# Performance work log

Hardware: AMD Instinct MI355X
Metric: run time of the kernel (lower is better)

The kernel has to match this reference:

```python
import jax, jax.numpy as jnp
import numpy as np

N = 20000      # nodes
E = 320000     # edges (before self loops)
HID = 128      # args.hidden
HEADS = 8
C1 = HID // 2  # 64, gat1 out per head -> 512 concat
C2 = HID // 4  # 32, gat2 out per head -> 256 concat
D1 = HEADS * C1  # 512
D2 = HEADS * C2  # 256
JKD = HID + D1 + D2  # 896


def _glorot(key, shape):
    fan_in, fan_out = shape[0], shape[-1]
    s = jnp.sqrt(6.0 / (fan_in + fan_out))
    return jax.random.uniform(key, shape, jnp.float32, -s, s)


def setup_inputs() -> dict:
    key = jax.random.key(0)
    ks = jax.random.split(key, 18)
    x = jax.random.normal(ks[0], (N, HID), jnp.float32)
    edge_index = jax.random.randint(ks[1], (2, E), 0, N, dtype=jnp.int32)
    return {
        "x": x,
        "edge_index": edge_index,
        # GATv2 layer 1
        "Wl1": _glorot(ks[2], (HID, D1)), "bl1": jnp.zeros((D1,), jnp.float32),
        "Wr1": _glorot(ks[3], (HID, D1)), "br1": jnp.zeros((D1,), jnp.float32),
        "att1": _glorot(ks[4], (HEADS, C1)),
        "bias1": jnp.zeros((D1,), jnp.float32),
        # GATv2 layer 2
        "Wl2": _glorot(ks[5], (D1, D2)), "bl2": jnp.zeros((D2,), jnp.float32),
        "Wr2": _glorot(ks[6], (D1, D2)), "br2": jnp.zeros((D2,), jnp.float32),
        "att2": _glorot(ks[7], (HEADS, C2)),
        "bias2": jnp.zeros((D2,), jnp.float32),
        # JK linear
        "Wjk": _glorot(ks[8], (JKD, HID)), "bjk": jnp.zeros((HID,), jnp.float32),
    }


def gatv2_layer(x, src, dst, Wl, bl, Wr, br, att, bias, n):
    """PyG GATv2Conv (concat=True, eval mode: no dropout), neg_slope=0.2."""
    H, C = att.shape
    xl = (x @ Wl + bl).reshape(n, H, C)  # source transform (messages)
    xr = (x @ Wr + br).reshape(n, H, C)  # target transform
    e = jax.nn.leaky_relu(xl[src] + xr[dst], 0.2)        # [E,H,C]
    logits = jnp.einsum('ehc,hc->eh', e, att)            # [E,H]
    # numerically stable segment softmax over incoming edges per dst node
    m = jax.ops.segment_max(logits, dst, num_segments=n) # [N,H]
    a = jnp.exp(logits - m[dst])
    denom = jax.ops.segment_sum(a, dst, num_segments=n)
    alpha = a / denom[dst]                               # [E,H]
    out = jax.ops.segment_sum(alpha[:, :, None] * xl[src], dst, num_segments=n)
    return out.reshape(n, H * C) + bias


def reference(x, edge_index, Wl1, bl1, Wr1, br1, att1, bias1,
              Wl2, bl2, Wr2, br2, att2, bias2, Wjk, bjk):
    n = x.shape[0]
    loop = jnp.arange(n, dtype=edge_index.dtype)
    src = jnp.concatenate([edge_index[0], loop])  # add self loops (PyG default)
    dst = jnp.concatenate([edge_index[1], loop])

    jk0 = x
    h1 = jax.nn.elu(gatv2_layer(x, src, dst, Wl1, bl1, Wr1, br1, att1, bias1, n))
    h2 = jax.nn.elu(gatv2_layer(h1, src, dst, Wl2, bl2, Wr2, br2, att2, bias2, n))
    jk = jnp.concatenate([jk0, h1, h2], axis=-1)  # JumpingKnowledge('cat')
    return jk @ Wjk + bjk
```

## Files before the change

### kernel.cpp

```cpp
#include <hip/hip_runtime.h>

typedef unsigned short u16;
typedef __attribute__((ext_vector_type(8))) short bf16x8;
typedef __attribute__((ext_vector_type(4))) float f32x4;

__device__ __forceinline__ float bf2f(u16 u) { return __uint_as_float(((unsigned)u) << 16); }
__device__ __forceinline__ u16 f2bf(float f) {
  unsigned u = __float_as_uint(f);
  u += 0x7fffu + ((u >> 16) & 1u);
  return (u16)(u >> 16);
}
__device__ __forceinline__ void bf2x2(unsigned w, float& lo, float& hi) {
  lo = __uint_as_float(w << 16);
  hi = __uint_as_float(w & 0xffff0000u);
}

__global__ __launch_bounds__(256) void prep_kernel(
    const float* __restrict__ x,
    const float* __restrict__ bl1, const float* __restrict__ br1,
    const float* __restrict__ bl2, const float* __restrict__ br2,
    u16* __restrict__ XH, float* __restrict__ BC1, float* __restrict__ BC2,
    int nx, int total)
{
  int i = blockIdx.x * 256 + threadIdx.x;
  if (i >= total) return;
  if (i < nx) { XH[i] = f2bf(x[i]); return; }
  int j = i - nx;
  if (j < 1024) { BC1[j] = (j < 512) ? bl1[j] : br1[j - 512]; return; }
  int t = j - 1024;
  BC2[t] = (t < 256) ? bl2[t] : br2[t - 256];
}

__global__ __launch_bounds__(256) void wtrans_kernel(
    const float* __restrict__ Wl1, const float* __restrict__ Wr1,
    const float* __restrict__ Wl2, const float* __restrict__ Wr2,
    const float* __restrict__ Wjk,
    u16* __restrict__ Wp)
{
  __shared__ float T[64][65];
  int t = blockIdx.x;
  const float *Wa, *Wb; int Nhalf, lds, k0, n0, KsT, SUBS; size_t obase; bool split;
  if (t < 32) {
    int kt = t & 1, nt = t >> 1;
    k0 = kt * 64; n0 = nt * 64; obase = 0; KsT = 4; SUBS = 8; split = true;
    Wa = Wl1; Wb = Wr1; Nhalf = 512; lds = 512;
  } else if (t < 96) {
    int tt = t - 32; int kt = tt & 7, nt = tt >> 3;
    k0 = kt * 64; n0 = nt * 64; obase = 262144; KsT = 16; SUBS = 8; split = true;
    Wa = Wl2; Wb = Wr2; Nhalf = 256; lds = 256;
  } else {
    int tt = t - 96; int kt = tt % 14, nt = tt / 14;
    k0 = kt * 64; n0 = nt * 64; obase = 786432; KsT = 28; SUBS = 4; split = false;
    Wa = Wjk; Wb = nullptr; Nhalf = 128; lds = 128;
  }
  const int tid = threadIdx.x;
  const int lane = tid & 63, unit = tid >> 6;
  {
    int n = n0 + lane;
    const float* S = (n < Nhalf) ? Wa : Wb;
    int nn = (n < Nhalf) ? n : n - Nhalf;
#pragma unroll
    for (int r = 0; r < 16; ++r) {
      int kl = unit + 4 * r;
      T[kl][lane] = S[(size_t)(k0 + kl) * lds + nn];
    }
  }
  __syncthreads();
  const int tn = n0 >> 6;
#pragma unroll
  for (int u = 0; u < 2; ++u) {
    int c = unit * 2 + u;
    int ks_l = c >> 2, nc = c & 3;
    int ksg = (k0 >> 5) + ks_l;
    size_t ob = obase + ((size_t)(tn * KsT + ksg) * SUBS + nc) * 512 + lane * 8;
#pragma unroll
    for (int j = 0; j < 8; ++j) {
      float v = T[ks_l * 32 + (lane >> 4) * 8 + j][nc * 16 + (lane & 15)];
      u16 h = f2bf(v);
      Wp[ob + j] = h;
      if (split) Wp[ob + 2048 + j] = f2bf(v - bf2f(h));
    }
  }
}

__global__ __launch_bounds__(256) void hist_kernel(
    const int* __restrict__ ei, int E, int ET, int* __restrict__ cnt)
{
  int e = blockIdx.x * 256 + threadIdx.x;
  if (e >= ET) return;
  int d = (e < E) ? ei[E + e] : (e - E);
  atomicAdd(&cnt[d], 1);
}

__global__ __launch_bounds__(1024) void scan_kernel(
    const int* __restrict__ cnt, int* __restrict__ rowptr, int n)
{
  __shared__ int wsum[16];
  __shared__ int carry;
  const int tid = threadIdx.x, lane = tid & 63, wv = tid >> 6;
  if (tid == 0) carry = 0;
  __syncthreads();
  for (int base = 0; base < n; base += 1024) {
    int i = base + tid;
    int v = (i < n) ? cnt[i] : 0;
    int s = v;
#pragma unroll
    for (int ofs = 1; ofs < 64; ofs <<= 1) {
      int t = __shfl_up(s, ofs);
      if (lane >= ofs) s += t;
    }
    if (lane == 63) wsum[wv] = s;
    __syncthreads();
    if (wv == 0 && lane < 16) {
      int t = wsum[lane];
#pragma unroll
      for (int ofs = 1; ofs < 16; ofs <<= 1) {
        int u = __shfl_up(t, ofs);
        if (lane >= ofs) t += u;
      }
      wsum[lane] = t;
    }
    __syncthreads();
    int waveoff = (wv == 0) ? 0 : wsum[wv - 1];
    if (i < n) rowptr[i] = carry + waveoff + s - v;
    int tot = wsum[15];
    __syncthreads();
    if (tid == 0) carry += tot;
    __syncthreads();
  }
  if (threadIdx.x == 0) rowptr[n] = carry;
}

__global__ __launch_bounds__(256) void scatter_kernel(
    const int* __restrict__ ei, int E, int ET,
    const int* __restrict__ rowptr, int* __restrict__ cur, int* __restrict__ srcs)
{
  int e = blockIdx.x * 256 + threadIdx.x;
  if (e >= ET) return;
  int s, d;
  if (e < E) { s = ei[e]; d = ei[E + e]; } else { s = e - E; d = s; }
  int pos = rowptr[d] + atomicAdd(&cur[d], 1);
  srcs[pos] = s;
}

template<int MROWS, int NW, int WPE, bool SPLIT, bool BF16OUT, int LDSU16>
__global__ __launch_bounds__(NW * 64, WPE) void gemmct_kernel(
    const u16* __restrict__ A0, int lda0, int K0,
    const u16* __restrict__ A1, int lda1, int K1,
    const u16* __restrict__ A2, int lda2, int K2,
    const u16* __restrict__ Wp, int KsT,
    int kof0, int kof1, int kof2,
    const float* __restrict__ bias,
    void* __restrict__ Cv, int ldc, int M, int N)
{
  constexpr int SUBS = SPLIT ? 8 : 4;
  __shared__ u16 ldsA[LDSU16];
  const int tid  = threadIdx.x;
  const int lane = tid & 63;
  const int wv   = tid >> 6;
  const int quad = lane >> 4;
  const int r16  = lane & 15;
  const int m0   = blockIdx.x * MROWS;

  const u16* As[3]   = {A0, A1, A2};
  const int  Ks[3]   = {K0, K1, K2};
  const int  ldas[3] = {lda0, lda1, lda2};
  const int  kofs[3] = {kof0, kof1, kof2};

  int soff[3];
  int so = 0;
#pragma unroll
  for (int s = 0; s < 3; ++s) {
    const int K = Ks[s];
    soff[s] = so;
    if (K == 0) continue;
    const int stride = K + 8;
    const int cpr = K >> 3;
    const int sh  = 32 - __clz(cpr - 1);
    const int tot = MROWS << sh;
    for (int c = tid; c < tot; c += NW * 64) {
      int row = c >> sh, kc = c & ((1 << sh) - 1);
      if (kc < cpr) {
        int sr = m0 + row; if (sr >= M) sr = M - 1;
        uint4 v = *reinterpret_cast<const uint4*>(As[s] + (size_t)sr * ldas[s] + kc * 8);
        *reinterpret_cast<uint4*>(&ldsA[so + row * stride + kc * 8]) = v;
      }
    }
    so += MROWS * stride;
  }
  __syncthreads();

  constexpr int MM = MROWS / 16;
  for (int n0w = wv * 64; n0w < N; n0w += NW * 64) {
    const int t = n0w >> 6;
    f32x4 acc[MM][4];
#pragma unroll
    for (int mm = 0; mm < MM; ++mm)
#pragma unroll
      for (int nc = 0; nc < 4; ++nc) acc[mm][nc] = (f32x4){0.f, 0.f, 0.f, 0.f};

#pragma unroll
    for (int s = 0; s < 3; ++s) {
      const int K = Ks[s];
      if (K == 0) continue;
      const int stride = K + 8;
      const int ksb = kofs[s] >> 5;
      const u16* lbase = &ldsA[soff[s] + r16 * stride + quad * 8];

#pragma unroll 2
      for (int k0 = 0; k0 < K; k0 += 32) {
        const int ks = ksb + (k0 >> 5);
        const u16* ch = Wp + (((size_t)(t * KsT + ks) * SUBS) << 9) + lane * 8;
        bf16x8 af[MM];
#pragma unroll
        for (int mm = 0; mm < MM; ++mm)
          af[mm] = *reinterpret_cast<const bf16x8*>(lbase + mm * 16 * stride + k0);
        bf16x8 whf[4], wlf[4];
#pragma unroll
        for (int nc = 0; nc < 4; ++nc) {
          whf[nc] = *reinterpret_cast<const bf16x8*>(ch + (nc << 9));
          if (SPLIT) wlf[nc] = *reinterpret_cast<const bf16x8*>(ch + ((4 + nc) << 9));
        }
#pragma unroll
        for (int mm = 0; mm < MM; ++mm)
#pragma unroll
          for (int nc = 0; nc < 4; ++nc) {
            acc[mm][nc] = __builtin_amdgcn_mfma_f32_16x16x32_bf16(whf[nc], af[mm], acc[mm][nc], 0, 0, 0);
            if (SPLIT)
              acc[mm][nc] = __builtin_amdgcn_mfma_f32_16x16x32_bf16(wlf[nc], af[mm], acc[mm][nc], 0, 0, 0);
          }
      }
    }

#pragma unroll
    for (int mm = 0; mm < MM; ++mm) {
      const int m = m0 + mm * 16 + r16;
      if (m >= M) continue;
#pragma unroll
      for (int nc = 0; nc < 4; ++nc) {
        const int n = n0w + nc * 16 + quad * 4;
        float b0 = 0.f, b1 = 0.f, b2 = 0.f, b3 = 0.f;
        if (bias) {
          float4 bv = *reinterpret_cast<const float4*>(bias + n);
          b0 = bv.x; b1 = bv.y; b2 = bv.z; b3 = bv.w;
        }
        float v0 = acc[mm][nc][0] + b0;
        float v1 = acc[mm][nc][1] + b1;
        float v2 = acc[mm][nc][2] + b2;
        float v3 = acc[mm][nc][3] + b3;
        if (BF16OUT) {
          ushort4 o = { f2bf(v0), f2bf(v1), f2bf(v2), f2bf(v3) };
          *reinterpret_cast<ushort4*>((u16*)Cv + (size_t)m * ldc + n) = o;
        } else {
          float4 o = { v0, v1, v2, v3 };
          *reinterpret_cast<float4*>((float*)Cv + (size_t)m * ldc + n) = o;
        }
      }
    }
  }
}

template<int VPL>
__device__ __forceinline__ void load_row(const u16* p, float* dst) {
  if constexpr (VPL == 8) {
    uint4 t = *reinterpret_cast<const uint4*>(p);
    bf2x2(t.x, dst[0], dst[1]); bf2x2(t.y, dst[2], dst[3]);
    bf2x2(t.z, dst[4], dst[5]); bf2x2(t.w, dst[6], dst[7]);
  } else {
    uint2 t = *reinterpret_cast<const uint2*>(p);
    bf2x2(t.x, dst[0], dst[1]); bf2x2(t.y, dst[2], dst[3]);
  }
}

template<int C>
__global__ __launch_bounds__(256) void gat_node_kernel(
    const u16* __restrict__ XLR,
    const int* __restrict__ rowptr, const int* __restrict__ srcs,
    const float* __restrict__ att, const float* __restrict__ bias,
    u16* __restrict__ Hh, int Nn)
{
  constexpr int D = C * 8;
  constexpr int VPL = D / 64;
  const int lane = threadIdx.x & 63;
  const int wv  = (blockIdx.x * 256 + threadIdx.x) >> 6;
  const int nwv = (gridDim.x * 256) >> 6;

  float c1[VPL], c2[VPL], biasR[VPL];
#pragma unroll
  for (int w = 0; w < VPL; ++w) {
    float a = att[lane * VPL + w];
    c1[w] = 0.6f * a;
    c2[w] = 0.4f * a;
    biasR[w] = bias[lane * VPL + w];
  }

  for (int d = wv; d < Nn; d += nwv) {
    float xr[VPL];
    load_row<VPL>(XLR + (size_t)d * (2 * D) + D + lane * VPL, xr);

    const int jb = rowptr[d], je = rowptr[d + 1];

    float acc[VPL];
    load_row<VPL>(XLR + (size_t)srcs[jb] * (2 * D) + lane * VPL, acc);
    float p0 = 0.f;
#pragma unroll
    for (int w = 0; w < VPL; ++w) {
      float v = acc[w] + xr[w];
      p0 = fmaf(c1[w], v, fmaf(c2[w], fabsf(v), p0));
    }
    p0 += __shfl_xor(p0, 1);
    p0 += __shfl_xor(p0, 2);
    p0 += __shfl_xor(p0, 4);
    float den = 1.f;

    int j = jb + 1;
    for (; j + 3 < je; j += 4) {
      float xa[VPL], xb[VPL], xc[VPL], xd[VPL];
      load_row<VPL>(XLR + (size_t)srcs[j]     * (2 * D) + lane * VPL, xa);
      load_row<VPL>(XLR + (size_t)srcs[j + 1] * (2 * D) + lane * VPL, xb);
      load_row<VPL>(XLR + (size_t)srcs[j + 2] * (2 * D) + lane * VPL, xc);
      load_row<VPL>(XLR + (size_t)srcs[j + 3] * (2 * D) + lane * VPL, xd);
      float pa = 0.f, pb = 0.f, pc = 0.f, pd = 0.f;
#pragma unroll
      for (int w = 0; w < VPL; ++w) {
        float va = xa[w] + xr[w];
        float vb = xb[w] + xr[w];
        float vc = xc[w] + xr[w];
        float vd = xd[w] + xr[w];
        pa = fmaf(c1[w], va, fmaf(c2[w], fabsf(va), pa));
        pb = fmaf(c1[w], vb, fmaf(c2[w], fabsf(vb), pb));
        pc = fmaf(c1[w], vc, fmaf(c2[w], fabsf(vc), pc));
        pd = fmaf(c1[w], vd, fmaf(c2[w], fabsf(vd), pd));
      }
      pa += __shfl_xor(pa, 1); pb += __shfl_xor(pb, 1);
      pc += __shfl_xor(pc, 1); pd += __shfl_xor(pd, 1);
      pa += __shfl_xor(pa, 2); pb += __shfl_xor(pb, 2);
      pc += __shfl_xor(pc, 2); pd += __shfl_xor(pd, 2);
      pa += __shfl_xor(pa, 4); pb += __shfl_xor(pb, 4);
      pc += __shfl_xor(pc, 4); pd += __shfl_xor(pd, 4);
      const float ea = __expf(pa - p0);
      const float eb = __expf(pb - p0);
      const float ec = __expf(pc - p0);
      const float ed = __expf(pd - p0);
      den += (ea + eb) + (ec + ed);
#pragma unroll
      for (int w = 0; w < VPL; ++w) {
        float t0 = fmaf(ea, xa[w], fmaf(eb, xb[w], acc[w]));
        acc[w] = fmaf(ec, xc[w], fmaf(ed, xd[w], t0));
      }
    }
    if (j + 1 < je) {
      float xa[VPL], xb[VPL];
      load_row<VPL>(XLR + (size_t)srcs[j]     * (2 * D) + lane * VPL, xa);
      load_row<VPL>(XLR + (size_t)srcs[j + 1] * (2 * D) + lane * VPL, xb);
      float pa = 0.f, pb = 0.f;
#pragma unroll
      for (int w = 0; w < VPL; ++w) {
        float va = xa[w] + xr[w];
        float vb = xb[w] + xr[w];
        pa = fmaf(c1[w], va, fmaf(c2[w], fabsf(va), pa));
        pb = fmaf(c1[w], vb, fmaf(c2[w], fabsf(vb), pb));
      }
      pa += __shfl_xor(pa, 1); pb += __shfl_xor(pb, 1);
      pa += __shfl_xor(pa, 2); pb += __shfl_xor(pb, 2);
      pa += __shfl_xor(pa, 4); pb += __shfl_xor(pb, 4);
      const float ea = __expf(pa - p0);
      const float eb = __expf(pb - p0);
      den += ea + eb;
#pragma unroll
      for (int w = 0; w < VPL; ++w)
        acc[w] = fmaf(ea, xa[w], fmaf(eb, xb[w], acc[w]));
      j += 2;
    }
    if (j < je) {
      float xa[VPL];
      load_row<VPL>(XLR + (size_t)srcs[j] * (2 * D) + lane * VPL, xa);
      float pa = 0.f;
#pragma unroll
      for (int w = 0; w < VPL; ++w) {
        float va = xa[w] + xr[w];
        pa = fmaf(c1[w], va, fmaf(c2[w], fabsf(va), pa));
      }
      pa += __shfl_xor(pa, 1);
      pa += __shfl_xor(pa, 2);
      pa += __shfl_xor(pa, 4);
      const float ea = __expf(pa - p0);
      den += ea;
#pragma unroll
      for (int w = 0; w < VPL; ++w) acc[w] = fmaf(ea, xa[w], acc[w]);
    }

    const float inv = 1.f / den;
    u16* hh = Hh + (size_t)d * D + lane * VPL;
#pragma unroll
    for (int w = 0; w < VPL; ++w) {
      float v = fmaf(acc[w], inv, biasR[w]);
      v = v > 0.f ? v : (__expf(v) - 1.f);
      hh[w] = f2bf(v);
    }
  }
}


extern "C" void kernel_launch(void* const* d_in, const int* in_sizes, int n_in,
                              void* d_out, int out_size, void* d_ws, size_t ws_size,
                              hipStream_t stream) {
  const float* x     = (const float*)d_in[0];
  const int*   ei    = (const int*)d_in[1];
  const float* Wl1   = (const float*)d_in[2];
  const float* bl1   = (const float*)d_in[3];
  const float* Wr1   = (const float*)d_in[4];
  const float* br1   = (const float*)d_in[5];
  const float* att1  = (const float*)d_in[6];
  const float* bias1 = (const float*)d_in[7];
  const float* Wl2   = (const float*)d_in[8];
  const float* bl2   = (const float*)d_in[9];
  const float* Wr2   = (const float*)d_in[10];
  const float* br2   = (const float*)d_in[11];
  const float* att2  = (const float*)d_in[12];
  const float* bias2 = (const float*)d_in[13];
  const float* Wjk   = (const float*)d_in[14];
  const float* bjk   = (const float*)d_in[15];
  float* out = (float*)d_out;

  const int Nn = in_sizes[0] / 128;
  const int E  = in_sizes[1] / 2;
  const int ET = E + Nn;

  const size_t nx = (size_t)Nn * 128;

  const size_t oW1  = 0;
  const size_t oW2  = 262144;
  const size_t oWjk = 786432;
  const size_t npack = 901120;

  char* ws = (char*)d_ws;
  size_t off = 0;
  u16* XH = (u16*)(ws + off); off += nx * 2;
  u16* Wp = (u16*)(ws + off); off += npack * 2;
  float* BC1 = (float*)(ws + off); off += 1024 * 4;
  float* BC2 = (float*)(ws + off); off += 512 * 4;
  u16* XLR1 = (u16*)(ws + off);
  u16* XLR2 = XLR1;
  off += (size_t)Nn * 1024 * 2;
  u16* H1h = (u16*)(ws + off); off += (size_t)Nn * 512 * 2;
  u16* H2h = (u16*)(ws + off); off += (size_t)Nn * 256 * 2;
  int* rowptr = (int*)(ws + off); off += (size_t)(Nn + 1) * 4;
  int* cur    = (int*)(ws + off); off += (size_t)Nn * 4;
  int* srcs   = (int*)(ws + off); off += (size_t)ET * 4;

  const int nodeblocks = 5000;

  const int nprep = (int)(nx + 1536);
  prep_kernel<<<(nprep + 255) / 256, 256, 0, stream>>>(
      x, bl1, br1, bl2, br2, XH, BC1, BC2, (int)nx, nprep);
  wtrans_kernel<<<124, 256, 0, stream>>>(Wl1, Wr1, Wl2, Wr2, Wjk, Wp);
  hipMemsetAsync(cur, 0, (size_t)Nn * 4, stream);
  hist_kernel<<<(ET + 255) / 256, 256, 0, stream>>>(ei, E, ET, cur);
  scan_kernel<<<1, 1024, 0, stream>>>(cur, rowptr, Nn);
  hipMemsetAsync(cur, 0, (size_t)Nn * 4, stream);
  scatter_kernel<<<(ET + 255) / 256, 256, 0, stream>>>(ei, E, ET, rowptr, cur, srcs);

  gemmct_kernel<32, 8, 4, true, true, 32 * 136>
      <<<(Nn + 31) / 32, 512, 0, stream>>>(
      XH, 128, 128, nullptr, 0, 0, nullptr, 0, 0,
      Wp + oW1, 4, 0, 0, 0, BC1,
      XLR1, 1024, Nn, 1024);
  gat_node_kernel<64><<<nodeblocks, 256, 0, stream>>>(
      XLR1, rowptr, srcs, att1, bias1, H1h, Nn);

  gemmct_kernel<48, 8, 4, true, true, 48 * 520>
      <<<(Nn + 47) / 48, 512, 0, stream>>>(
      H1h, 512, 512, nullptr, 0, 0, nullptr, 0, 0,
      Wp + oW2, 16, 0, 0, 0, BC2,
      XLR2, 512, Nn, 512);
  gat_node_kernel<32><<<nodeblocks, 256, 0, stream>>>(
      XLR2, rowptr, srcs, att2, bias2, H2h, Nn);

  gemmct_kernel<16, 2, 1, false, false, 16 * 920>
      <<<(Nn + 15) / 16, 128, 0, stream>>>(
      XH, 128, 128, H1h, 512, 512, H2h, 256, 256,
      Wp + oWjk, 28, 0, 128, 640, bjk,
      out, 128, Nn, 128);
}
```

Measured before the change: 321.3 us.

## Fuse prep/weight/scatter launches and split GAT aggregation per head

Merges the prep and weight-transpose kernels into one launch that also zeroes the degree counters. The scan now resets the counters itself, and the edge scatter runs as extra blocks inside the first GEMM launch. Together these remove two memsets and two kernel launches. The GAT aggregation kernels are rewritten so that each block handles one head and each node is processed by a small group of 8 or 4 lanes rather than a whole wave, using ds_swizzle reductions and packed 16-byte stores. The tradeoff is more per-node divergence within a wave and repeated rowptr/srcs reads once per head.

After: 298.9 us. 7.0% less time.

```diff
diff --git a/kernel.cpp b/kernel.cpp
--- a/kernel.cpp
+++ b/kernel.cpp
@@ -14,31 +14,45 @@
   lo = __uint_as_float(w << 16);
   hi = __uint_as_float(w & 0xffff0000u);
 }
-
-__global__ __launch_bounds__(256) void prep_kernel(
+__device__ __forceinline__ unsigned pk2(float lo, float hi) {
+  return (unsigned)f2bf(lo) | ((unsigned)f2bf(hi) << 16);
+}
+
+__device__ __forceinline__ float red8(float p) {
+  p += __int_as_float(__builtin_amdgcn_ds_swizzle(__float_as_int(p), 0x041F));
+  p += __int_as_float(__builtin_amdgcn_ds_swizzle(__float_as_int(p), 0x081F));
+  p += __int_as_float(__builtin_amdgcn_ds_swizzle(__float_as_int(p), 0x101F));
+  return p;
+}
+__device__ __forceinline__ float red4(float p) {
+  p += __int_as_float(__builtin_amdgcn_ds_swizzle(__float_as_int(p), 0x041F));
+  p += __int_as_float(__builtin_amdgcn_ds_swizzle(__float_as_int(p), 0x081F));
+  return p;
+}
+
+__global__ __launch_bounds__(256) void prepw_kernel(
     const float* __restrict__ x,
     const float* __restrict__ bl1, const float* __restrict__ br1,
     const float* __restrict__ bl2, const float* __restrict__ br2,
-    u16* __restrict__ XH, float* __restrict__ BC1, float* __restrict__ BC2,
-    int nx, int total)
-{
-  int i = blockIdx.x * 256 + threadIdx.x;
-  if (i >= total) return;
-  if (i < nx) { XH[i] = f2bf(x[i]); return; }
-  int j = i - nx;
-  if (j < 1024) { BC1[j] = (j < 512) ? bl1[j] : br1[j - 512]; return; }
-  int t = j - 1024;
-  BC2[t] = (t < 256) ? bl2[t] : br2[t - 256];
-}
-
-__global__ __launch_bounds__(256) void wtrans_kernel(
     const float* __restrict__ Wl1, const float* __restrict__ Wr1,
     const float* __restrict__ Wl2, const float* __restrict__ Wr2,
     const float* __restrict__ Wjk,
-    u16* __restrict__ Wp)
-{
+    u16* __restrict__ XH, float* __restrict__ BC1, float* __restrict__ BC2,
+    int* __restrict__ cur, u16* __restrict__ Wp,
+    int nx, int total, int prepBlocks)
+{
+  if (blockIdx.x < prepBlocks) {
+    int i = blockIdx.x * 256 + threadIdx.x;
+    if (i >= total) return;
+    if (i < nx) { XH[i] = f2bf(x[i]); return; }
+    int j = i - nx;
+    if (j < 1024) { BC1[j] = (j < 512) ? bl1[j] : br1[j - 512]; return; }
+    if (j < 1536) { int t = j - 1024; BC2[t] = (t < 256) ? bl2[t] : br2[t - 256]; return; }
+    cur[j - 1536] = 0;
+    return;
+  }
   __shared__ float T[64][65];
-  int t = blockIdx.x;
+  int t = blockIdx.x - prepBlocks;
   const float *Wa, *Wb; int Nhalf, lds, k0, n0, KsT, SUBS; size_t obase; bool split;
   if (t < 32) {
     int kt = t & 1, nt = t >> 1;
@@ -93,7 +107,7 @@
 }
 
 __global__ __launch_bounds__(1024) void scan_kernel(
-    const int* __restrict__ cnt, int* __restrict__ rowptr, int n)
+    int* __restrict__ cnt, int* __restrict__ rowptr, int n)
 {
   __shared__ int wsum[16];
   __shared__ int carry;
@@ -103,6 +117,7 @@
   for (int base = 0; base < n; base += 1024) {
     int i = base + tid;
     int v = (i < n) ? cnt[i] : 0;
+    if (i < n) cnt[i] = 0;
     int s = v;
 #pragma unroll
     for (int ofs = 1; ofs < 64; ofs <<= 1) {
@@ -131,20 +146,9 @@
   if (threadIdx.x == 0) rowptr[n] = carry;
 }
 
-__global__ __launch_bounds__(256) void scatter_kernel(
-    const int* __restrict__ ei, int E, int ET,
-    const int* __restrict__ rowptr, int* __restrict__ cur, int* __restrict__ srcs)
-{
-  int e = blockIdx.x * 256 + threadIdx.x;
-  if (e >= ET) return;
-  int s, d;
-  if (e < E) { s = ei[e]; d = ei[E + e]; } else { s = e - E; d = s; }
-  int pos = rowptr[d] + atomicAdd(&cur[d], 1);
-  srcs[pos] = s;
-}
-
-template<int MROWS, int NW, int WPE, bool SPLIT, bool BF16OUT, int LDSU16>
-__global__ __launch_bounds__(NW * 64, WPE) void gemmct_kernel(
+template<int MROWS, int NW, bool SPLIT, bool BF16OUT>
+__device__ __forceinline__ void gemmct_body(
+    u16* __restrict__ ldsA, int bid,
     const u16* __restrict__ A0, int lda0, int K0,
     const u16* __restrict__ A1, int lda1, int K1,
     const u16* __restrict__ A2, int lda2, int K2,
@@ -154,13 +158,12 @@
     void* __restrict__ Cv, int ldc, int M, int N)
 {
   constexpr int SUBS = SPLIT ? 8 : 4;
-  __shared__ u16 ldsA[LDSU16];
   const int tid  = threadIdx.x;
   const int lane = tid & 63;
   const int wv   = tid >> 6;
   const int quad = lane >> 4;
   const int r16  = lane & 15;
-  const int m0   = blockIdx.x * MROWS;
+  const int m0   = bid * MROWS;
 
   const u16* As[3]   = {A0, A1, A2};
   const int  Ks[3]   = {K0, K1, K2};
@@ -260,6 +263,46 @@
   }
 }
 
+template<int MROWS, int NW, int WPE, bool SPLIT, bool BF16OUT, int LDSU16>
+__global__ __launch_bounds__(NW * 64, WPE) void gemmct_kernel(
+    const u16* __restrict__ A0, int lda0, int K0,
+    const u16* __restrict__ A1, int lda1, int K1,
+    const u16* __restrict__ A2, int lda2, int K2,
+    const u16* __restrict__ Wp, int KsT,
+    int kof0, int kof1, int kof2,
+    const float* __restrict__ bias,
+    void* __restrict__ Cv, int ldc, int M, int N)
+{
+  __shared__ u16 ldsA[LDSU16];
+  gemmct_body<MROWS, NW, SPLIT, BF16OUT>(
+      ldsA, blockIdx.x, A0, lda0, K0, A1, lda1, K1, A2, lda2, K2,
+      Wp, KsT, kof0, kof1, kof2, bias, Cv, ldc, M, N);
+}
+
+template<int MROWS, int NW, int WPE, bool SPLIT, bool BF16OUT, int LDSU16>
+__global__ __launch_bounds__(NW * 64, WPE) void gemm1_scatter_kernel(
+    const u16* __restrict__ A0, int lda0, int K0,
+    const u16* __restrict__ Wp, int KsT,
+    const float* __restrict__ bias,
+    void* __restrict__ Cv, int ldc, int M, int N, int gemmBlocks,
+    const int* __restrict__ ei, int E, int ET,
+    const int* __restrict__ rowptr, int* __restrict__ cur, int* __restrict__ srcs)
+{
+  __shared__ u16 ldsA[LDSU16];
+  if ((int)blockIdx.x < gemmBlocks) {
+    gemmct_body<MROWS, NW, SPLIT, BF16OUT>(
+        ldsA, blockIdx.x, A0, lda0, K0, nullptr, 0, 0, nullptr, 0, 0,
+        Wp, KsT, 0, 0, 0, bias, Cv, ldc, M, N);
+    return;
+  }
+  int e = ((int)blockIdx.x - gemmBlocks) * (NW * 64) + (int)threadIdx.x;
+  if (e >= ET) return;
+  int s, d;
+  if (e < E) { s = ei[e]; d = ei[E + e]; } else { s = e - E; d = s; }
+  int pos = rowptr[d] + atomicAdd(&cur[d], 1);
+  srcs[pos] = s;
+}
+
 template<int VPL>
 __device__ __forceinline__ void load_row(const u16* p, float* dst) {
   if constexpr (VPL == 8) {
@@ -272,132 +315,181 @@
   }
 }
 
-template<int C>
-__global__ __launch_bounds__(256) void gat_node_kernel(
+__global__ __launch_bounds__(256) void gath1_kernel(
     const u16* __restrict__ XLR,
     const int* __restrict__ rowptr, const int* __restrict__ srcs,
     const float* __restrict__ att, const float* __restrict__ bias,
     u16* __restrict__ Hh, int Nn)
 {
-  constexpr int D = C * 8;
-  constexpr int VPL = D / 64;
-  const int lane = threadIdx.x & 63;
-  const int wv  = (blockIdx.x * 256 + threadIdx.x) >> 6;
-  const int nwv = (gridDim.x * 256) >> 6;
-
-  float c1[VPL], c2[VPL], biasR[VPL];
-#pragma unroll
-  for (int w = 0; w < VPL; ++w) {
-    float a = att[lane * VPL + w];
+  const int tid   = threadIdx.x;
+  const int s     = tid & 7;
+  const int gib   = tid >> 3;
+  const int head  = blockIdx.x & 7;
+  const int chunk = blockIdx.x >> 3;
+  const int nch   = gridDim.x >> 3;
+
+  const int hoff = head * 64 + s * 8;
+
+  float c1[8], c2[8], biasR[8];
+#pragma unroll
+  for (int w = 0; w < 8; ++w) {
+    float a = att[hoff + w];
     c1[w] = 0.6f * a;
     c2[w] = 0.4f * a;
-    biasR[w] = bias[lane * VPL + w];
-  }
-
-  for (int d = wv; d < Nn; d += nwv) {
-    float xr[VPL];
-    load_row<VPL>(XLR + (size_t)d * (2 * D) + D + lane * VPL, xr);
-
+    biasR[w] = bias[hoff + w];
+  }
+
+  for (int d = chunk * 32 + gib; d < Nn; d += nch * 32) {
+    float xr[8];
+    load_row<8>(XLR + (size_t)d * 1024 + 512 + hoff, xr);
     const int jb = rowptr[d], je = rowptr[d + 1];
 
-    float acc[VPL];
-    load_row<VPL>(XLR + (size_t)srcs[jb] * (2 * D) + lane * VPL, acc);
+    float acc[8];
+    load_row<8>(XLR + (size_t)srcs[jb] * 1024 + hoff, acc);
     float p0 = 0.f;
 #pragma unroll
-    for (int w = 0; w < VPL; ++w) {
+    for (int w = 0; w < 8; ++w) {
       float v = acc[w] + xr[w];
       p0 = fmaf(c1[w], v, fmaf(c2[w], fabsf(v), p0));
     }
-    p0 += __shfl_xor(p0, 1);
-    p0 += __shfl_xor(p0, 2);
-    p0 += __shfl_xor(p0, 4);
+    p0 = red8(p0);
     float den = 1.f;
 
     int j = jb + 1;
-    for (; j + 3 < je; j += 4) {
-      float xa[VPL], xb[VPL], xc[VPL], xd[VPL];
-      load_row<VPL>(XLR + (size_t)srcs[j]     * (2 * D) + lane * VPL, xa);
-      load_row<VPL>(XLR + (size_t)srcs[j + 1] * (2 * D) + lane * VPL, xb);
-      load_row<VPL>(XLR + (size_t)srcs[j + 2] * (2 * D) + lane * VPL, xc);
-      load_row<VPL>(XLR + (size_t)srcs[j + 3] * (2 * D) + lane * VPL, xd);
-      float pa = 0.f, pb = 0.f, pc = 0.f, pd = 0.f;
-#pragma unroll
-      for (int w = 0; w < VPL; ++w) {
-        float va = xa[w] + xr[w];
-        float vb = xb[w] + xr[w];
-        float vc = xc[w] + xr[w];
-        float vd = xd[w] + xr[w];
-        pa = fmaf(c1[w], va, fmaf(c2[w], fabsf(va), pa));
-        pb = fmaf(c1[w], vb, fmaf(c2[w], fabsf(vb), pb));
-        pc = fmaf(c1[w], vc, fmaf(c2[w], fabsf(vc), pc));
-        pd = fmaf(c1[w], vd, fmaf(c2[w], fabsf(vd), pd));
-      }
-      pa += __shfl_xor(pa, 1); pb += __shfl_xor(pb, 1);
-      pc += __shfl_xor(pc, 1); pd += __shfl_xor(pd, 1);
-      pa += __shfl_xor(pa, 2); pb += __shfl_xor(pb, 2);
-      pc += __shfl_xor(pc, 2); pd += __shfl_xor(pd, 2);
-      pa += __shfl_xor(pa, 4); pb += __shfl_xor(pb, 4);
-      pc += __shfl_xor(pc, 4); pd += __shfl_xor(pd, 4);
-      const float ea = __expf(pa - p0);
-      const float eb = __expf(pb - p0);
-      const float ec = __expf(pc - p0);
-      const float ed = __expf(pd - p0);
-      den += (ea + eb) + (ec + ed);
-#pragma unroll
-      for (int w = 0; w < VPL; ++w) {
-        float t0 = fmaf(ea, xa[w], fmaf(eb, xb[w], acc[w]));
-        acc[w] = fmaf(ec, xc[w], fmaf(ed, xd[w], t0));
-      }
-    }
-    if (j + 1 < je) {
-      float xa[VPL], xb[VPL];
-      load_row<VPL>(XLR + (size_t)srcs[j]     * (2 * D) + lane * VPL, xa);
-      load_row<VPL>(XLR + (size_t)srcs[j + 1] * (2 * D) + lane * VPL, xb);
+    for (; j + 1 < je; j += 2) {
+      float xa[8], xb[8];
+      load_row<8>(XLR + (size_t)srcs[j]     * 1024 + hoff, xa);
+      load_row<8>(XLR + (size_t)srcs[j + 1] * 1024 + hoff, xb);
       float pa = 0.f, pb = 0.f;
 #pragma unroll
-      for (int w = 0; w < VPL; ++w) {
+      for (int w = 0; w < 8; ++w) {
         float va = xa[w] + xr[w];
         float vb = xb[w] + xr[w];
         pa = fmaf(c1[w], va, fmaf(c2[w], fabsf(va), pa));
         pb = fmaf(c1[w], vb, fmaf(c2[w], fabsf(vb), pb));
       }
-      pa += __shfl_xor(pa, 1); pb += __shfl_xor(pb, 1);
-      pa += __shfl_xor(pa, 2); pb += __shfl_xor(pb, 2);
-      pa += __shfl_xor(pa, 4); pb += __shfl_xor(pb, 4);
+      pa = red8(pa); pb = red8(pb);
       const float ea = __expf(pa - p0);
       const float eb = __expf(pb - p0);
       den += ea + eb;
 #pragma unroll
-      for (int w = 0; w < VPL; ++w)
+      for (int w = 0; w < 8; ++w)
         acc[w] = fmaf(ea, xa[w], fmaf(eb, xb[w], acc[w]));
-      j += 2;
     }
     if (j < je) {
-      float xa[VPL];
-      load_row<VPL>(XLR + (size_t)srcs[j] * (2 * D) + lane * VPL, xa);
+      float xa[8];
+      load_row<8>(XLR + (size_t)srcs[j] * 1024 + hoff, xa);
       float pa = 0.f;
 #pragma unroll
-      for (int w = 0; w < VPL; ++w) {
+      for (int w = 0; w < 8; ++w) {
         float va = xa[w] + xr[w];
         pa = fmaf(c1[w], va, fmaf(c2[w], fabsf(va), pa));
       }
-      pa += __shfl_xor(pa, 1);
-      pa += __shfl_xor(pa, 2);
-      pa += __shfl_xor(pa, 4);
+      pa = red8(pa);
       const float ea = __expf(pa - p0);
       den += ea;
 #pragma unroll
-      for (int w = 0; w < VPL; ++w) acc[w] = fmaf(ea, xa[w], acc[w]);
+      for (int w = 0; w < 8; ++w) acc[w] = fmaf(ea, xa[w], acc[w]);
     }
 
     const float inv = 1.f / den;
-    u16* hh = Hh + (size_t)d * D + lane * VPL;
-#pragma unroll
-    for (int w = 0; w < VPL; ++w) {
+    float o[8];
+#pragma unroll
+    for (int w = 0; w < 8; ++w) {
       float v = fmaf(acc[w], inv, biasR[w]);
-      v = v > 0.f ? v : (__expf(v) - 1.f);
-      hh[w] = f2bf(v);
-    }
+      o[w] = v > 0.f ? v : (__expf(v) - 1.f);
+    }
+    uint4 ov = { pk2(o[0], o[1]), pk2(o[2], o[3]), pk2(o[4], o[5]), pk2(o[6], o[7]) };
+    *reinterpret_cast<uint4*>(Hh + (size_t)d * 512 + hoff) = ov;
+  }
+}
+
+__global__ __launch_bounds__(256) void gath2_kernel(
+    const u16* __restrict__ XLR,
+    const int* __restrict__ rowptr, const int* __restrict__ srcs,
+    const float* __restrict__ att, const float* __restrict__ bias,
+    u16* __restrict__ Hh, int Nn)
+{
+  const int tid   = threadIdx.x;
+  const int s     = tid & 3;
+  const int gib   = tid >> 2;
+  const int head  = blockIdx.x & 7;
+  const int chunk = blockIdx.x >> 3;
+  const int nch   = gridDim.x >> 3;
+
+  const int hoff = head * 32 + s * 8;
+
+  float c1[8], c2[8], biasR[8];
+#pragma unroll
+  for (int w = 0; w < 8; ++w) {
+    float a = att[hoff + w];
+    c1[w] = 0.6f * a;
+    c2[w] = 0.4f * a;
+    biasR[w] = bias[hoff + w];
+  }
+
+  for (int d = chunk * 64 + gib; d < Nn; d += nch * 64) {
+    float xr[8];
+    load_row<8>(XLR + (size_t)d * 512 + 256 + hoff, xr);
+    const int jb = rowptr[d], je = rowptr[d + 1];
+
+    float acc[8];
+    load_row<8>(XLR + (size_t)srcs[jb] * 512 + hoff, acc);
+    float p0 = 0.f;
+#pragma unroll
+    for (int w = 0; w < 8; ++w) {
+      float v = acc[w] + xr[w];
+      p0 = fmaf(c1[w], v, fmaf(c2[w], fabsf(v), p0));
+    }
+    p0 = red4(p0);
+    float den = 1.f;
+
+    int j = jb + 1;
+    for (; j + 1 < je; j += 2) {
+      float xa[8], xb[8];
+      load_row<8>(XLR + (size_t)srcs[j]     * 512 + hoff, xa);
+      load_row<8>(XLR + (size_t)srcs[j + 1] * 512 + hoff, xb);
+      float pa = 0.f, pb = 0.f;
+#pragma unroll
+      for (int w = 0; w < 8; ++w) {
+        float va = xa[w] + xr[w];
+        float vb = xb[w] + xr[w];
+        pa = fmaf(c1[w], va, fmaf(c2[w], fabsf(va), pa));
+        pb = fmaf(c1[w], vb, fmaf(c2[w], fabsf(vb), pb));
+      }
+      pa = red4(pa); pb = red4(pb);
+      const float ea = __expf(pa - p0);
+      const float eb = __expf(pb - p0);
+      den += ea + eb;
+#pragma unroll
+      for (int w = 0; w < 8; ++w)
+        acc[w] = fmaf(ea, xa[w], fmaf(eb, xb[w], acc[w]));
+    }
+    if (j < je) {
+      float xa[8];
+      load_row<8>(XLR + (size_t)srcs[j] * 512 + hoff, xa);
+      float pa = 0.f;
+#pragma unroll
+      for (int w = 0; w < 8; ++w) {
+        float va = xa[w] + xr[w];
+        pa = fmaf(c1[w], va, fmaf(c2[w], fabsf(va), pa));
+      }
+      pa = red4(pa);
+      const float ea = __expf(pa - p0);
+      den += ea;
+#pragma unroll
+      for (int w = 0; w < 8; ++w) acc[w] = fmaf(ea, xa[w], acc[w]);
+    }
+
+    const float inv = 1.f / den;
+    float o[8];
+#pragma unroll
+    for (int w = 0; w < 8; ++w) {
+      float v = fmaf(acc[w], inv, biasR[w]);
+      o[w] = v > 0.f ? v : (__expf(v) - 1.f);
+    }
+    uint4 ov = { pk2(o[0], o[1]), pk2(o[2], o[3]), pk2(o[4], o[5]), pk2(o[6], o[7]) };
+    *reinterpret_cast<uint4*>(Hh + (size_t)d * 256 + hoff) = ov;
   }
 }
 
@@ -449,24 +541,23 @@
   int* cur    = (int*)(ws + off); off += (size_t)Nn * 4;
   int* srcs   = (int*)(ws + off); off += (size_t)ET * 4;
 
-  const int nodeblocks = 5000;
-
-  const int nprep = (int)(nx + 1536);
-  prep_kernel<<<(nprep + 255) / 256, 256, 0, stream>>>(
-      x, bl1, br1, bl2, br2, XH, BC1, BC2, (int)nx, nprep);
-  wtrans_kernel<<<124, 256, 0, stream>>>(Wl1, Wr1, Wl2, Wr2, Wjk, Wp);
-  hipMemsetAsync(cur, 0, (size_t)Nn * 4, stream);
+  const int nprep = (int)(nx + 1536 + Nn);
+  const int prepBlocks = (nprep + 255) / 256;
+  prepw_kernel<<<prepBlocks + 124, 256, 0, stream>>>(
+      x, bl1, br1, bl2, br2, Wl1, Wr1, Wl2, Wr2, Wjk,
+      XH, BC1, BC2, cur, Wp, (int)nx, nprep, prepBlocks);
   hist_kernel<<<(ET + 255) / 256, 256, 0, stream>>>(ei, E, ET, cur);
   scan_kernel<<<1, 1024, 0, stream>>>(cur, rowptr, Nn);
-  hipMemsetAsync(cur, 0, (size_t)Nn * 4, stream);
-  scatter_kernel<<<(ET + 255) / 256, 256, 0, stream>>>(ei, E, ET, rowptr, cur, srcs);
-
-  gemmct_kernel<32, 8, 4, true, true, 32 * 136>
-      <<<(Nn + 31) / 32, 512, 0, stream>>>(
-      XH, 128, 128, nullptr, 0, 0, nullptr, 0, 0,
-      Wp + oW1, 4, 0, 0, 0, BC1,
-      XLR1, 1024, Nn, 1024);
-  gat_node_kernel<64><<<nodeblocks, 256, 0, stream>>>(
+
+  const int g1blocks = (Nn + 31) / 32;
+  const int scatBlocks = (ET + 511) / 512;
+  gemm1_scatter_kernel<32, 8, 4, true, true, 32 * 136>
+      <<<g1blocks + scatBlocks, 512, 0, stream>>>(
+      XH, 128, 128,
+      Wp + oW1, 4, BC1,
+      XLR1, 1024, Nn, 1024, g1blocks,
+      ei, E, ET, rowptr, cur, srcs);
+  gath1_kernel<<<5000, 256, 0, stream>>>(
       XLR1, rowptr, srcs, att1, bias1, H1h, Nn);
 
   gemmct_kernel<48, 8, 4, true, true, 48 * 520>
@@ -474,7 +565,7 @@
       H1h, 512, 512, nullptr, 0, 0, nullptr, 0, 0,
       Wp + oW2, 16, 0, 0, 0, BC2,
       XLR2, 512, Nn, 512);
-  gat_node_kernel<32><<<nodeblocks, 256, 0, stream>>>(
+  gath2_kernel<<<2504, 256, 0, stream>>>(
       XLR2, rowptr, srcs, att2, bias2, H2h, Nn);
 
   gemmct_kernel<16, 2, 1, false, false, 16 * 920>
```
